# Performance work log

Measured on AMD Instinct MI355X. Metric: run time of the kernel, lower is better.

The kernel has to match this reference:

```python
import jax, jax.numpy as jnp
import numpy as np

B, IN, H = 16384, 1024, 1024


def setup_inputs() -> dict:
    key = jax.random.key(0)
    ks = jax.random.split(key, 16)
    stdv = 1.0 / np.sqrt(H)
    u = lambda k, shape: jax.random.uniform(k, shape, jnp.float32, -stdv, stdv)
    return {
        "input": jax.random.normal(ks[0], (B, IN), jnp.float32),
        "prev_h": jax.random.normal(ks[1], (B, H), jnp.float32),
        "prev_c": jax.random.normal(ks[2], (B, H), jnp.float32),
        "weight_xi": u(ks[3], (IN, H)), "weight_hi": u(ks[4], (H, H)),
        "weight_xf": u(ks[5], (IN, H)), "weight_hf": u(ks[6], (H, H)),
        "weight_xu": u(ks[7], (IN, H)), "weight_hu": u(ks[8], (H, H)),
        "weight_xo": u(ks[9], (IN, H)), "weight_ho": u(ks[10], (H, H)),
        "bias_i": u(ks[11], (H,)), "bias_f": u(ks[12], (H,)),
        "bias_o": u(ks[13], (H,)), "bias_u": u(ks[14], (H,)),
    }


def reference(input, prev_h, prev_c,
              weight_xi, weight_hi, weight_xf, weight_hf,
              weight_xu, weight_hu, weight_xo, weight_ho,
              bias_i, bias_f, bias_o, bias_u):
    i = jax.nn.sigmoid(input @ weight_xi + prev_h @ weight_hi + bias_i)
    f = jax.nn.sigmoid(input @ weight_xf + prev_h @ weight_hf + bias_f)
    o = jax.nn.sigmoid(input @ weight_xo + prev_h @ weight_ho + bias_o)
    u = jnp.tanh(input @ weight_xu + prev_h @ weight_hu + bias_u)
    c = f * prev_c + i * u
    h = o * jnp.tanh(c)
    return (h, c)
```

## Files before the change

kernel.cpp:

```cpp
#include <hip/hip_runtime.h>
#include <hip/hip_bf16.h>
#include <stdint.h>
#include <type_traits>


typedef short bf16x8 __attribute__((ext_vector_type(8)));
typedef unsigned short u16x8 __attribute__((ext_vector_type(8)));
typedef float f32x4 __attribute__((ext_vector_type(4)));

__device__ __forceinline__ unsigned short f2bf(float f) {
    union { float f; uint32_t u; } v; v.f = f;
    uint32_t r = v.u + 0x7FFFu + ((v.u >> 16) & 1u);
    return (unsigned short)(r >> 16);
}

__device__ __forceinline__ float fsig(float x) { return 1.0f / (1.0f + __expf(-x)); }
__device__ __forceinline__ float ftanh(float x) { return 2.0f * fsig(2.0f * x) - 1.0f; }

__global__ __launch_bounds__(256) void pack_a_kernel(const float* __restrict__ input,
                                                     const float* __restrict__ prev_h,
                                                     unsigned short* __restrict__ Apk) {
    long idx = (long)blockIdx.x * 256 + threadIdx.x;
    long e0 = idx * 8;
    int b = (int)(e0 >> 11);
    int k = (int)(e0 & 2047);
    const float* src = (k < 1024) ? (input + (size_t)b * 1024 + k)
                                  : (prev_h + (size_t)b * 1024 + (k - 1024));
    float4 lo = *(const float4*)src;
    float4 hi = *(const float4*)(src + 4);
    u16x8 o;
    o[0] = f2bf(lo.x); o[1] = f2bf(lo.y); o[2] = f2bf(lo.z); o[3] = f2bf(lo.w);
    o[4] = f2bf(hi.x); o[5] = f2bf(hi.y); o[6] = f2bf(hi.z); o[7] = f2bf(hi.w);
    *(u16x8*)(Apk + e0) = o;
}

__global__ __launch_bounds__(256) void pack_b_kernel(
        const float* __restrict__ wxi, const float* __restrict__ wxf,
        const float* __restrict__ wxo, const float* __restrict__ wxu,
        const float* __restrict__ whi, const float* __restrict__ whf,
        const float* __restrict__ who, const float* __restrict__ whu,
        unsigned short* __restrict__ Bpk) {
    int idx = blockIdx.x * 256 + threadIdx.x;
    int g  = idx >> 18;
    int r  = idx & 262143;
    int kc = r >> 10;
    int j  = r & 1023;
    const float* wx = (g == 0) ? wxi : (g == 1) ? wxf : (g == 2) ? wxo : wxu;
    const float* wh = (g == 0) ? whi : (g == 1) ? whf : (g == 2) ? who : whu;
    int k0 = kc * 8;
    const float* src = (k0 < 1024) ? (wx + (size_t)k0 * 1024 + j)
                                   : (wh + (size_t)(k0 - 1024) * 1024 + j);
    u16x8 o;
#pragma unroll
    for (int t = 0; t < 8; ++t) o[t] = f2bf(src[(size_t)t * 1024]);
    *(u16x8*)(Bpk + (((size_t)(g * 1024 + j)) << 11) + k0) = o;
}


#define GLL(gp, lp) __builtin_amdgcn_global_load_lds( \
        (__attribute__((address_space(1))) void*)(gp), \
        (__attribute__((address_space(3))) void*)(lp), 16, 0, 0)

#define BAR() do { asm volatile("" ::: "memory"); __builtin_amdgcn_s_barrier(); \
                   asm volatile("" ::: "memory"); } while (0)

__global__ __launch_bounds__(512, 2) void lstm_gemm_kernel(
        const unsigned short* __restrict__ Apk,
        const unsigned short* __restrict__ Bpk,
        const float* __restrict__ prev_c,
        const float* __restrict__ bi, const float* __restrict__ bf_,
        const float* __restrict__ bo, const float* __restrict__ bu,
        float* __restrict__ out_h, float* __restrict__ out_c) {
    __shared__ __align__(16) unsigned char smem[131072];
    const int tid = threadIdx.x;
    const int w = tid >> 6, l = tid & 63;
    const int lr = l & 15, s4 = l >> 4;
    const int wm = w >> 2, wq = w & 3;

    const int bid = blockIdx.x;
    const int sw = ((bid & 7) << 7) + (bid >> 3);
    const int tileRow = sw & 63, tileCol = sw >> 6;
    const int rowBase = tileRow * 256;
    const int jBase = tileCol * 64;

    const int swr = ((s4 ^ ((lr >> 1) & 3)) << 4);

    int aoff[8], boff[4];
#pragma unroll
    for (int m = 0; m < 8; ++m) aoff[m] = (wm * 128 + m * 16 + lr) * 64 + swr;
#pragma unroll
    for (int g = 0; g < 4; ++g) boff[g] = 16384 + (g * 64 + wq * 16 + lr) * 64 + swr;

    const int slot = (l & 3) ^ ((l >> 3) & 3);
    const int rloc = w * 16 + (l >> 2);
    const unsigned short* aSrc0 = Apk + (size_t)(rowBase + rloc) * 2048 + slot * 8;
    const unsigned short* aSrc1 = Apk + (size_t)(rowBase + 128 + rloc) * 2048 + slot * 8;
    const int br0 = rloc, br1 = 128 + rloc;
    const unsigned short* bSrc0 = Bpk + (((size_t)((br0 >> 6) * 1024 + jBase + (br0 & 63))) << 11) + slot * 8;
    const unsigned short* bSrc1 = Bpk + (((size_t)((br1 >> 6) * 1024 + jBase + (br1 & 63))) << 11) + slot * 8;
    const int aDst0 = w * 1024;
    const int aDst1 = 8192 + w * 1024;
    const int bDst0 = 16384 + w * 1024;
    const int bDst1 = 24576 + w * 1024;

#define STAGE_A(BUFB, T) do { \
        GLL(aSrc0 + (size_t)(T) * 32, smem + (BUFB) + aDst0); \
        GLL(aSrc1 + (size_t)(T) * 32, smem + (BUFB) + aDst1); } while (0)
#define STAGE_B(BUFB, T) do { \
        GLL(bSrc0 + (size_t)(T) * 32, smem + (BUFB) + bDst0); \
        GLL(bSrc1 + (size_t)(T) * 32, smem + (BUFB) + bDst1); } while (0)

    f32x4 acc[8][4];
    const f32x4 vzero = {0.f, 0.f, 0.f, 0.f};
#pragma unroll
    for (int m = 0; m < 8; ++m)
#pragma unroll
        for (int g = 0; g < 4; ++g) acc[m][g] = vzero;

    STAGE_A(0, 0);      STAGE_B(0, 0);
    STAGE_A(32768, 1);  STAGE_B(32768, 1);
    STAGE_A(65536, 2);  STAGE_B(65536, 2);
    asm volatile("s_waitcnt vmcnt(8)" ::: "memory");
    BAR();

    auto ktile = [&](int t, auto vnc, auto stgc) {
        constexpr int VN = decltype(vnc)::value;
        constexpr bool STG = decltype(stgc)::value;
        const int bt = (t & 3) * 32768;
        const int b3 = ((t + 3) & 3) * 32768;
        bf16x8 av[4], bv[4];
#pragma unroll
        for (int m = 0; m < 4; ++m) av[m] = *(const bf16x8*)(smem + bt + aoff[m]);
#pragma unroll
        for (int g = 0; g < 4; ++g) bv[g] = *(const bf16x8*)(smem + bt + boff[g]);
        if constexpr (STG) STAGE_A(b3, t + 3);
        BAR();
        __builtin_amdgcn_s_setprio(1);
#pragma unroll
        for (int m = 0; m < 4; ++m)
#pragma unroll
            for (int g = 0; g < 4; ++g)
                acc[m][g] = __builtin_amdgcn_mfma_f32_16x16x32_bf16(av[m], bv[g], acc[m][g], 0, 0, 0);
        __builtin_amdgcn_s_setprio(0);
        BAR();
        bf16x8 av2[4];
#pragma unroll
        for (int m = 0; m < 4; ++m) av2[m] = *(const bf16x8*)(smem + bt + aoff[4 + m]);
        if constexpr (STG) STAGE_B(b3, t + 3);
        BAR();
        __builtin_amdgcn_s_setprio(1);
#pragma unroll
        for (int m = 0; m < 4; ++m)
#pragma unroll
            for (int g = 0; g < 4; ++g)
                acc[4 + m][g] = __builtin_amdgcn_mfma_f32_16x16x32_bf16(av2[m], bv[g], acc[4 + m][g], 0, 0, 0);
        __builtin_amdgcn_s_setprio(0);
        if constexpr (VN == 8) asm volatile("s_waitcnt vmcnt(8)" ::: "memory");
        else if constexpr (VN == 4) asm volatile("s_waitcnt vmcnt(4)" ::: "memory");
        else if constexpr (VN == 0) asm volatile("s_waitcnt vmcnt(0)" ::: "memory");
        if constexpr (VN >= 0) BAR();
    };

    using ci8 = std::integral_constant<int, 8>;
    using ci4 = std::integral_constant<int, 4>;
    using ci0 = std::integral_constant<int, 0>;
    using cim = std::integral_constant<int, -1>;
    using bt_ = std::integral_constant<bool, true>;
    using bf_c = std::integral_constant<bool, false>;

#pragma unroll 1
    for (int t = 0; t < 61; ++t) ktile(t, ci8{}, bt_{});
    ktile(61, ci4{}, bf_c{});
    ktile(62, ci0{}, bf_c{});
    ktile(63, cim{}, bf_c{});

    const int colIdx = jBase + wq * 16 + lr;
    const float vbi = bi[colIdx], vbf = bf_[colIdx], vbo = bo[colIdx], vbu = bu[colIdx];
    const int rowB = rowBase + wm * 128 + s4 * 4;
#pragma unroll
    for (int m = 0; m < 8; ++m) {
#pragma unroll
        for (int tt = 0; tt < 4; ++tt) {
            const size_t idx = (size_t)(rowB + m * 16 + tt) * 1024 + colIdx;
            float zi = acc[m][0][tt] + vbi;
            float zf = acc[m][1][tt] + vbf;
            float zo = acc[m][2][tt] + vbo;
            float zu = acc[m][3][tt] + vbu;
            float iv = fsig(zi), fv = fsig(zf), ov = fsig(zo), uv = ftanh(zu);
            float cv = fv * prev_c[idx] + iv * uv;
            out_c[idx] = cv;
            out_h[idx] = ov * ftanh(cv);
        }
    }
#undef STAGE_A
#undef STAGE_B
}

extern "C" void kernel_launch(void* const* d_in, const int* in_sizes, int n_in,
                              void* d_out, int out_size, void* d_ws, size_t ws_size,
                              hipStream_t stream) {
    const float* input  = (const float*)d_in[0];
    const float* prev_h = (const float*)d_in[1];
    const float* prev_c = (const float*)d_in[2];
    const float* wxi = (const float*)d_in[3];
    const float* whi = (const float*)d_in[4];
    const float* wxf = (const float*)d_in[5];
    const float* whf = (const float*)d_in[6];
    const float* wxu = (const float*)d_in[7];
    const float* whu = (const float*)d_in[8];
    const float* wxo = (const float*)d_in[9];
    const float* who = (const float*)d_in[10];
    const float* bi  = (const float*)d_in[11];
    const float* bf_ = (const float*)d_in[12];
    const float* bo  = (const float*)d_in[13];
    const float* bu  = (const float*)d_in[14];

    unsigned short* Apk = (unsigned short*)d_ws;
    unsigned short* Bpk = (unsigned short*)((char*)d_ws + (size_t)67108864);

    float* out_h = (float*)d_out;
    float* out_c = out_h + (size_t)16384 * 1024;

    pack_a_kernel<<<dim3(16384), dim3(256), 0, stream>>>(input, prev_h, Apk);
    pack_b_kernel<<<dim3(4096), dim3(256), 0, stream>>>(wxi, wxf, wxo, wxu,
                                                        whi, whf, who, whu, Bpk);
    lstm_gemm_kernel<<<dim3(1024), dim3(512), 0, stream>>>(Apk, Bpk, prev_c,
                                                           bi, bf_, bo, bu, out_h, out_c);
}
```

Measured before the change: 351.2 us.

## Double-buffer MFMA fragments in registers and cut barriers to one per k-tile

Restructures the k-loop so each iteration issues all global-to-LDS loads for tile t+3 at once. It then waits once, hits a single barrier, and prefetches the next tile's full A/B fragments into a second register buffer while running all 32 MFMAs on the current fragments. The loop is unrolled by two with ping-pong fragment arrays, and sched_group_barrier hints interleave the LDS reads with the MFMAs. The aim is to remove two of the three barriers per tile and hide LDS read latency behind matrix math. The cost is 24 extra live bf16x8 registers on top of a 128-register accumulator under a 512x2 launch bound, which risks spilling or lost occupancy.

```diff
diff --git a/kernel.cpp b/kernel.cpp
--- a/kernel.cpp
+++ b/kernel.cpp
@@ -61,9 +61,6 @@
         (__attribute__((address_space(1))) void*)(gp), \
         (__attribute__((address_space(3))) void*)(lp), 16, 0, 0)
 
-#define BAR() do { asm volatile("" ::: "memory"); __builtin_amdgcn_s_barrier(); \
-                   asm volatile("" ::: "memory"); } while (0)
-
 __global__ __launch_bounds__(512, 2) void lstm_gemm_kernel(
         const unsigned short* __restrict__ Apk,
         const unsigned short* __restrict__ Bpk,
@@ -103,12 +100,11 @@
     const int bDst0 = 16384 + w * 1024;
     const int bDst1 = 24576 + w * 1024;
 
-#define STAGE_A(BUFB, T) do { \
-        GLL(aSrc0 + (size_t)(T) * 32, smem + (BUFB) + aDst0); \
-        GLL(aSrc1 + (size_t)(T) * 32, smem + (BUFB) + aDst1); } while (0)
-#define STAGE_B(BUFB, T) do { \
-        GLL(bSrc0 + (size_t)(T) * 32, smem + (BUFB) + bDst0); \
-        GLL(bSrc1 + (size_t)(T) * 32, smem + (BUFB) + bDst1); } while (0)
+#define STAGE(T) do { const int _bb = ((T) & 3) * 32768; \
+        GLL(aSrc0 + (size_t)(T) * 32, smem + _bb + aDst0); \
+        GLL(aSrc1 + (size_t)(T) * 32, smem + _bb + aDst1); \
+        GLL(bSrc0 + (size_t)(T) * 32, smem + _bb + bDst0); \
+        GLL(bSrc1 + (size_t)(T) * 32, smem + _bb + bDst1); } while (0)
 
     f32x4 acc[8][4];
     const f32x4 vzero = {0.f, 0.f, 0.f, 0.f};
@@ -117,48 +113,46 @@
 #pragma unroll
         for (int g = 0; g < 4; ++g) acc[m][g] = vzero;
 
-    STAGE_A(0, 0);      STAGE_B(0, 0);
-    STAGE_A(32768, 1);  STAGE_B(32768, 1);
-    STAGE_A(65536, 2);  STAGE_B(65536, 2);
+    bf16x8 fra[12], frb[12];
+
+    auto ldfr = [&](int t, bf16x8 (&dst)[12]) {
+        const int bn = (t & 3) * 32768;
+#pragma unroll
+        for (int m = 0; m < 8; ++m) dst[m] = *(const bf16x8*)(smem + bn + aoff[m]);
+#pragma unroll
+        for (int g = 0; g < 4; ++g) dst[8 + g] = *(const bf16x8*)(smem + bn + boff[g]);
+    };
+
+    STAGE(0); STAGE(1); STAGE(2);
     asm volatile("s_waitcnt vmcnt(8)" ::: "memory");
-    BAR();
-
-    auto ktile = [&](int t, auto vnc, auto stgc) {
+    __builtin_amdgcn_s_barrier();
+    asm volatile("" ::: "memory");
+    ldfr(0, fra);
+
+    auto body = [&](int t, auto vnc, auto stgc, bf16x8 (&cur)[12], bf16x8 (&nxt)[12]) {
         constexpr int VN = decltype(vnc)::value;
         constexpr bool STG = decltype(stgc)::value;
-        const int bt = (t & 3) * 32768;
-        const int b3 = ((t + 3) & 3) * 32768;
-        bf16x8 av[4], bv[4];
-#pragma unroll
-        for (int m = 0; m < 4; ++m) av[m] = *(const bf16x8*)(smem + bt + aoff[m]);
-#pragma unroll
-        for (int g = 0; g < 4; ++g) bv[g] = *(const bf16x8*)(smem + bt + boff[g]);
-        if constexpr (STG) STAGE_A(b3, t + 3);
-        BAR();
+        if constexpr (STG) STAGE(t + 3);
+        if constexpr (VN >= 0) {
+            if constexpr (VN == 8)      asm volatile("s_waitcnt vmcnt(8)" ::: "memory");
+            else if constexpr (VN == 4) asm volatile("s_waitcnt vmcnt(4)" ::: "memory");
+            else                        asm volatile("s_waitcnt vmcnt(0)" ::: "memory");
+            asm volatile("s_waitcnt lgkmcnt(0)" ::: "memory");
+            __builtin_amdgcn_s_barrier();
+            asm volatile("" ::: "memory");
+            ldfr(t + 1, nxt);
+        }
         __builtin_amdgcn_s_setprio(1);
 #pragma unroll
-        for (int m = 0; m < 4; ++m)
+        for (int m = 0; m < 8; ++m)
 #pragma unroll
             for (int g = 0; g < 4; ++g)
-                acc[m][g] = __builtin_amdgcn_mfma_f32_16x16x32_bf16(av[m], bv[g], acc[m][g], 0, 0, 0);
+                acc[m][g] = __builtin_amdgcn_mfma_f32_16x16x32_bf16(cur[m], cur[8 + g], acc[m][g], 0, 0, 0);
         __builtin_amdgcn_s_setprio(0);
-        BAR();
-        bf16x8 av2[4];
-#pragma unroll
-        for (int m = 0; m < 4; ++m) av2[m] = *(const bf16x8*)(smem + bt + aoff[4 + m]);
-        if constexpr (STG) STAGE_B(b3, t + 3);
-        BAR();
-        __builtin_amdgcn_s_setprio(1);
-#pragma unroll
-        for (int m = 0; m < 4; ++m)
-#pragma unroll
-            for (int g = 0; g < 4; ++g)
-                acc[4 + m][g] = __builtin_amdgcn_mfma_f32_16x16x32_bf16(av2[m], bv[g], acc[4 + m][g], 0, 0, 0);
-        __builtin_amdgcn_s_setprio(0);
-        if constexpr (VN == 8) asm volatile("s_waitcnt vmcnt(8)" ::: "memory");
-        else if constexpr (VN == 4) asm volatile("s_waitcnt vmcnt(4)" ::: "memory");
-        else if constexpr (VN == 0) asm volatile("s_waitcnt vmcnt(0)" ::: "memory");
-        if constexpr (VN >= 0) BAR();
+        if constexpr (VN >= 0) {
+            __builtin_amdgcn_sched_group_barrier(0x100, 12, 0);
+            __builtin_amdgcn_sched_group_barrier(0x8,   32, 0);
+        }
     };
 
     using ci8 = std::integral_constant<int, 8>;
@@ -169,10 +163,14 @@
     using bf_c = std::integral_constant<bool, false>;
 
 #pragma unroll 1
-    for (int t = 0; t < 61; ++t) ktile(t, ci8{}, bt_{});
-    ktile(61, ci4{}, bf_c{});
-    ktile(62, ci0{}, bf_c{});
-    ktile(63, cim{}, bf_c{});
+    for (int t = 0; t < 60; t += 2) {
+        body(t,     ci8{}, bt_{}, fra, frb);
+        body(t + 1, ci8{}, bt_{}, frb, fra);
+    }
+    body(60, ci8{}, bt_{},  fra, frb);
+    body(61, ci4{}, bf_c{}, frb, fra);
+    body(62, ci0{}, bf_c{}, fra, frb);
+    body(63, cim{}, bf_c{}, frb, fra);
 
     const int colIdx = jBase + wq * 16 + lr;
     const float vbi = bi[colIdx], vbf = bf_[colIdx], vbo = bo[colIdx], vbu = bu[colIdx];
@@ -192,8 +190,7 @@
             out_h[idx] = ov * ftanh(cv);
         }
     }
-#undef STAGE_A
-#undef STAGE_B
+#undef STAGE
 }
 
 extern "C" void kernel_launch(void* const* d_in, const int* in_sizes, int n_in,
```

Result: no change. 351.3 us (+0.0%).

## Shorten GEMM prefetch to depth two and drop a barrier per k-tile

Applied to the files above, without the earlier changes.

Changes the K-loop pipeline from prefetching three tiles ahead to two, cutting one block barrier per k-tile and moving the vmcnt wait into the second half. It adds explicit lgkmcnt waits and sched_barriers before each MFMA batch, and unrolls the loop by two with alternating B register sets. The aim is lower synchronisation overhead and tighter scheduling of LDS reads against MFMA. The shallower prefetch may expose more global-load latency, and the four LDS buffers could see reuse hazards.

```diff
diff --git a/kernel.cpp b/kernel.cpp
--- a/kernel.cpp
+++ b/kernel.cpp
@@ -103,12 +103,12 @@
     const int bDst0 = 16384 + w * 1024;
     const int bDst1 = 24576 + w * 1024;
 
-#define STAGE_A(BUFB, T) do { \
-        GLL(aSrc0 + (size_t)(T) * 32, smem + (BUFB) + aDst0); \
-        GLL(aSrc1 + (size_t)(T) * 32, smem + (BUFB) + aDst1); } while (0)
-#define STAGE_B(BUFB, T) do { \
-        GLL(bSrc0 + (size_t)(T) * 32, smem + (BUFB) + bDst0); \
-        GLL(bSrc1 + (size_t)(T) * 32, smem + (BUFB) + bDst1); } while (0)
+#define STAGE_A2(T) do { const int _bb = ((T) & 3) * 32768; \
+        GLL(aSrc0 + (size_t)(T) * 32, smem + _bb + aDst0); \
+        GLL(aSrc1 + (size_t)(T) * 32, smem + _bb + aDst1); } while (0)
+#define STAGE_B2(T) do { const int _bb = ((T) & 3) * 32768; \
+        GLL(bSrc0 + (size_t)(T) * 32, smem + _bb + bDst0); \
+        GLL(bSrc1 + (size_t)(T) * 32, smem + _bb + bDst1); } while (0)
 
     f32x4 acc[8][4];
     const f32x4 vzero = {0.f, 0.f, 0.f, 0.f};
@@ -117,51 +117,51 @@
 #pragma unroll
         for (int g = 0; g < 4; ++g) acc[m][g] = vzero;
 
-    STAGE_A(0, 0);      STAGE_B(0, 0);
-    STAGE_A(32768, 1);  STAGE_B(32768, 1);
-    STAGE_A(65536, 2);  STAGE_B(65536, 2);
-    asm volatile("s_waitcnt vmcnt(8)" ::: "memory");
+    bf16x8 bvA[4], bvB[4];
+
+    STAGE_A2(0); STAGE_B2(0);
+    STAGE_A2(1); STAGE_B2(1);
+    asm volatile("s_waitcnt vmcnt(4)" ::: "memory");
     BAR();
 
-    auto ktile = [&](int t, auto vnc, auto stgc) {
+    auto slice = [&](int t, auto vnc, auto stgc, bf16x8 (&bv)[4]) {
         constexpr int VN = decltype(vnc)::value;
         constexpr bool STG = decltype(stgc)::value;
         const int bt = (t & 3) * 32768;
-        const int b3 = ((t + 3) & 3) * 32768;
-        bf16x8 av[4], bv[4];
-#pragma unroll
-        for (int m = 0; m < 4; ++m) av[m] = *(const bf16x8*)(smem + bt + aoff[m]);
+        bf16x8 av0[4];
+#pragma unroll
+        for (int m = 0; m < 4; ++m) av0[m] = *(const bf16x8*)(smem + bt + aoff[m]);
 #pragma unroll
         for (int g = 0; g < 4; ++g) bv[g] = *(const bf16x8*)(smem + bt + boff[g]);
-        if constexpr (STG) STAGE_A(b3, t + 3);
+        if constexpr (STG) STAGE_A2(t + 2);
         BAR();
+        asm volatile("s_waitcnt lgkmcnt(0)" ::: "memory");
+        __builtin_amdgcn_sched_barrier(0);
         __builtin_amdgcn_s_setprio(1);
 #pragma unroll
         for (int m = 0; m < 4; ++m)
 #pragma unroll
             for (int g = 0; g < 4; ++g)
-                acc[m][g] = __builtin_amdgcn_mfma_f32_16x16x32_bf16(av[m], bv[g], acc[m][g], 0, 0, 0);
+                acc[m][g] = __builtin_amdgcn_mfma_f32_16x16x32_bf16(av0[m], bv[g], acc[m][g], 0, 0, 0);
         __builtin_amdgcn_s_setprio(0);
+        bf16x8 av1[4];
+#pragma unroll
+        for (int m = 0; m < 4; ++m) av1[m] = *(const bf16x8*)(smem + bt + aoff[4 + m]);
+        if constexpr (STG) STAGE_B2(t + 2);
+        if constexpr (VN == 4)      asm volatile("s_waitcnt vmcnt(4)" ::: "memory");
+        else if constexpr (VN == 0) asm volatile("s_waitcnt vmcnt(0)" ::: "memory");
         BAR();
-        bf16x8 av2[4];
-#pragma unroll
-        for (int m = 0; m < 4; ++m) av2[m] = *(const bf16x8*)(smem + bt + aoff[4 + m]);
-        if constexpr (STG) STAGE_B(b3, t + 3);
-        BAR();
+        asm volatile("s_waitcnt lgkmcnt(0)" ::: "memory");
+        __builtin_amdgcn_sched_barrier(0);
         __builtin_amdgcn_s_setprio(1);
 #pragma unroll
         for (int m = 0; m < 4; ++m)
 #pragma unroll
             for (int g = 0; g < 4; ++g)
-                acc[4 + m][g] = __builtin_amdgcn_mfma_f32_16x16x32_bf16(av2[m], bv[g], acc[4 + m][g], 0, 0, 0);
+                acc[4 + m][g] = __builtin_amdgcn_mfma_f32_16x16x32_bf16(av1[m], bv[g], acc[4 + m][g], 0, 0, 0);
         __builtin_amdgcn_s_setprio(0);
-        if constexpr (VN == 8) asm volatile("s_waitcnt vmcnt(8)" ::: "memory");
-        else if constexpr (VN == 4) asm volatile("s_waitcnt vmcnt(4)" ::: "memory");
-        else if constexpr (VN == 0) asm volatile("s_waitcnt vmcnt(0)" ::: "memory");
-        if constexpr (VN >= 0) BAR();
     };
 
-    using ci8 = std::integral_constant<int, 8>;
     using ci4 = std::integral_constant<int, 4>;
     using ci0 = std::integral_constant<int, 0>;
     using cim = std::integral_constant<int, -1>;
@@ -169,10 +169,14 @@
     using bf_c = std::integral_constant<bool, false>;
 
 #pragma unroll 1
-    for (int t = 0; t < 61; ++t) ktile(t, ci8{}, bt_{});
-    ktile(61, ci4{}, bf_c{});
-    ktile(62, ci0{}, bf_c{});
-    ktile(63, cim{}, bf_c{});
+    for (int t = 0; t < 60; t += 2) {
+        slice(t,     ci4{}, bt_{}, bvA);
+        slice(t + 1, ci4{}, bt_{}, bvB);
+    }
+    slice(60, ci4{}, bt_{},  bvA);
+    slice(61, ci4{}, bt_{},  bvB);
+    slice(62, ci0{}, bf_c{}, bvA);
+    slice(63, cim{}, bf_c{}, bvB);
 
     const int colIdx = jBase + wq * 16 + lr;
     const float vbi = bi[colIdx], vbf = bf_[colIdx], vbo = bo[colIdx], vbu = bu[colIdx];
@@ -192,8 +196,8 @@
             out_h[idx] = ov * ftanh(cv);
         }
     }
-#undef STAGE_A
-#undef STAGE_B
+#undef STAGE_A2
+#undef STAGE_B2
 }
 
 extern "C" void kernel_launch(void* const* d_in, const int* in_sizes, int n_in,
```

Result: no change. 350.5 us (-0.2%).
